# Kernel tuning notes

Hardware: AMD Instinct MI355X
Metric: run time of the kernel (lower is better)

Reference implementation:

```python
import jax, jax.numpy as jnp
import numpy as np

# LIF neuron constants (standard mem_update)
THRESH = 0.5
LENS = 0.5
DECAY = 0.25
EPS = 1e-5
NUM_HEADS = 8

@jax.custom_vjp
def act_fun(mem):
    return (mem > THRESH).astype(mem.dtype)

def _act_fwd(mem):
    return act_fun(mem), mem

def _act_bwd(mem, g):
    surrogate = (jnp.abs(mem - THRESH) < LENS).astype(g.dtype)
    return (g * surrogate,)

act_fun.defvjp(_act_fwd, _act_bwd)

def mem_update(x):
    # x: (T, ...) -> binary spikes (T, ...) via recurrent LIF dynamics
    def step(carry, xt):
        mem_old, spike = carry
        # spike is detached in the reset gate (torch .detach())
        mem = mem_old * DECAY * (1.0 - jax.lax.stop_gradient(spike)) + xt
        s = act_fun(mem)
        return (mem, s), s
    init = (jnp.zeros_like(x[0]), jnp.zeros_like(x[0]))
    _, out = jax.lax.scan(step, init, x)
    return out

def bn(x, gamma, beta, mean, var):
    # inference-mode BatchNorm1d over channel dim of (T,B,C,L)
    inv = gamma / jnp.sqrt(var + EPS)
    return x * inv[None, None, :, None] + (beta - mean * inv)[None, None, :, None]

def setup_inputs() -> dict:
    key = jax.random.key(0)
    ks = jax.random.split(key, 11)
    T, B, C, L = 4, 2, 384, 1024
    s = 1.0 / np.sqrt(C)
    return {
        "x": jax.random.normal(ks[0], (T, B, C, L), jnp.float32),
        "W_w": jax.random.normal(ks[1], (2 * C, C), jnp.float32) * s,
        "bn1_gamma": jax.random.uniform(ks[2], (2 * C,), jnp.float32, 0.5, 1.5),
        "bn1_beta": jax.random.normal(ks[3], (2 * C,), jnp.float32) * 0.1,
        "bn1_mean": jax.random.normal(ks[4], (2 * C,), jnp.float32) * 0.1,
        "bn1_var": jax.random.uniform(ks[5], (2 * C,), jnp.float32, 0.5, 1.5),
        "proj_w": jax.random.normal(ks[6], (C, C), jnp.float32) * s,
        "bn2_gamma": jax.random.uniform(ks[7], (C,), jnp.float32, 0.5, 1.5),
        "bn2_beta": jax.random.normal(ks[8], (C,), jnp.float32) * 0.1,
        "bn2_mean": jax.random.normal(ks[9], (C,), jnp.float32) * 0.1,
        "bn2_var": jax.random.uniform(ks[10], (C,), jnp.float32, 0.5, 1.5),
    }

def reference(x, W_w, bn1_gamma, bn1_beta, bn1_mean, bn1_var, proj_w, bn2_gamma, bn2_beta, bn2_mean, bn2_var):
    T, B, C, L = x.shape
    H = NUM_HEADS
    d = C // H
    x_feat = x
    xs = mem_update(x)                                   # binary spikes (T,B,C,L)
    y = jnp.einsum('oc,tbcl->tbol', W_w, xs)             # 1x1 conv C->2C
    y = bn(y, bn1_gamma, bn1_beta, bn1_mean, bn1_var)
    y = y.reshape(T, B, H, 2 * d, L)
    y1, y2 = y[:, :, :, :d, :], y[:, :, :, d:, :]
    xr = xs.reshape(T, B, H, d, L)
    attn = jnp.einsum('tbhdl,tbhdm->tbhlm', y1, xr)      # (L,L) per head
    attn = mem_update(attn)                              # binary spikes
    out = jnp.einsum('tbhdl,tbhlm->tbhdm', y2, attn)
    out = out.reshape(T, B, C, L)
    out = mem_update(out)
    out = jnp.einsum('oc,tbcl->tbol', proj_w, out)       # Wproj 1x1
    out = bn(out, bn2_gamma, bn2_beta, bn2_mean, bn2_var)
    return out + x_feat
```

## Files before the change

kernel.cpp:

```cpp
#include <hip/hip_runtime.h>

#define T_  4
#define B_  2
#define C_  384
#define L_  1024
#define H_  8
#define C2_ 768
#define S_  (B_*C_*L_)

typedef __attribute__((ext_vector_type(8))) short short8;
typedef __attribute__((ext_vector_type(4))) float floatx4;
typedef __attribute__((ext_vector_type(16))) float floatx16;

__device__ __forceinline__ unsigned bf16_rne(float v) {
    unsigned u = __float_as_uint(v);
    u += 0x7FFFu + ((u >> 16) & 1u);
    return u >> 16;
}
__device__ __forceinline__ float bf16_to_f(unsigned h) { return __uint_as_float(h << 16); }
__device__ __forceinline__ void split3(float v, unsigned& hi, unsigned& mi, unsigned& lo) {
    hi = bf16_rne(v);
    float r1 = v - bf16_to_f(hi);
    mi = bf16_rne(r1);
    float r2 = r1 - bf16_to_f(mi);
    lo = bf16_rne(r2);
}

__global__ __launch_bounds__(256) void split_w(const float* __restrict__ W, int n4,
                                               unsigned short* __restrict__ hi,
                                               unsigned short* __restrict__ mi,
                                               unsigned short* __restrict__ lo) {
    int i = blockIdx.x * 256 + threadIdx.x;
    if (i >= n4) return;
    float4 v = ((const float4*)W)[i];
    float vv[4] = {v.x, v.y, v.z, v.w};
    union { unsigned short us[4]; uint2 u2; } h, m, l;
#pragma unroll
    for (int e = 0; e < 4; e++) {
        unsigned hh, mm, ll; split3(vv[e], hh, mm, ll);
        h.us[e] = (unsigned short)hh; m.us[e] = (unsigned short)mm; l.us[e] = (unsigned short)ll;
    }
    ((uint2*)hi)[i] = h.u2; ((uint2*)mi)[i] = m.u2; ((uint2*)lo)[i] = l.u2;
}

__global__ __launch_bounds__(256) void scan_transpose(const float* __restrict__ src,
                                                      unsigned short* __restrict__ dstT) {
    __shared__ unsigned short tile[64][72];
    const int tid = threadIdx.x;
    const int l0 = blockIdx.x * 64, c0 = blockIdx.y * 64, b = blockIdx.z;
    const int row = tid >> 2, seg = tid & 3;
    float mem[16], sp[16];
#pragma unroll
    for (int e = 0; e < 16; e++) { mem[e] = 0.f; sp[e] = 0.f; }
    for (int t = 0; t < T_; t++) {
        const size_t base = ((size_t)((t*B_ + b)*C_ + c0 + row))*L_ + l0 + seg*16;
#pragma unroll
        for (int qq = 0; qq < 4; qq++) {
            float4 v = *(const float4*)(src + base + qq*4);
            float vv[4] = {v.x, v.y, v.z, v.w};
            unsigned bs[4];
#pragma unroll
            for (int s = 0; s < 4; s++) {
                int e = qq*4 + s;
                mem[e] = mem[e]*0.25f*(1.f - sp[e]) + vv[s];
                bool sb = mem[e] > 0.5f;
                sp[e] = sb ? 1.f : 0.f;
                bs[s] = sb ? 0x3F80u : 0u;
            }
            *(unsigned*)&tile[row][seg*16 + qq*4]     = bs[0] | (bs[1] << 16);
            *(unsigned*)&tile[row][seg*16 + qq*4 + 2] = bs[2] | (bs[3] << 16);
        }
        __syncthreads();
        {
            const int lr = tid >> 2, cs = tid & 3;
#pragma unroll
            for (int sub = 0; sub < 2; sub++) {
                unsigned wv[4];
#pragma unroll
                for (int p = 0; p < 4; p++) {
                    unsigned e0 = tile[cs*16 + sub*8 + p*2][lr];
                    unsigned e1 = tile[cs*16 + sub*8 + p*2 + 1][lr];
                    wv[p] = e0 | (e1 << 16);
                }
                uint4 o; o.x = wv[0]; o.y = wv[1]; o.z = wv[2]; o.w = wv[3];
                *(uint4*)(dstT + ((size_t)(t*B_ + b)*L_ + l0 + lr)*C_ + c0 + cs*16 + sub*8) = o;
            }
        }
        __syncthreads();
    }
}

__global__ __launch_bounds__(256) void gemm1_mfma(
    const unsigned short* __restrict__ whi, const unsigned short* __restrict__ wmi,
    const unsigned short* __restrict__ wlo, const unsigned short* __restrict__ xsT,
    const float* __restrict__ g, const float* __restrict__ be,
    const float* __restrict__ mn, const float* __restrict__ vr,
    unsigned short* __restrict__ y1hi, unsigned short* __restrict__ y1mi,
    unsigned short* __restrict__ y1lo,
    unsigned short* __restrict__ y2hi, unsigned short* __restrict__ y2mi,
    unsigned short* __restrict__ y2lo) {
    __shared__ unsigned short A_hi[96][40], A_mi[96][40], A_lo[96][40];
    __shared__ unsigned short B_s[128][40];
    __shared__ unsigned short epi1[128*56];
    __shared__ unsigned short epi2[48*136];
    const int tid = threadIdx.x;
    const int tb = blockIdx.y;
    const int mt = blockIdx.x >> 3, lt = blockIdx.x & 7;
    const int l0 = lt * 128;
    const int w = tid >> 6, lane = tid & 63;
    const int q = lane >> 4, n15 = lane & 15;
    const int mw = (w & 1) * 48, lw = (w >> 1) * 64;

    floatx4 acc[3][4];
#pragma unroll
    for (int i = 0; i < 3; i++)
#pragma unroll
        for (int j = 0; j < 4; j++) acc[i][j] = (floatx4){0.f,0.f,0.f,0.f};

    for (int ck = 0; ck < C_; ck += 32) {
#pragma unroll
        for (int p = 0; p < 3; p++) {
            const unsigned short* wp = p == 0 ? whi : p == 1 ? wmi : wlo;
            unsigned short (*ap)[40] = p == 0 ? A_hi : p == 1 ? A_mi : A_lo;
            for (int s = tid; s < 384; s += 256) {
                int r = s >> 2, c = s & 3;
                *(uint4*)&ap[r][c*8] = *(const uint4*)(wp + (size_t)(mt*96 + r)*C_ + ck + c*8);
            }
        }
        for (int s = tid; s < 512; s += 256) {
            int r = s >> 2, c4 = s & 3;
            *(uint4*)&B_s[r][c4*8] = *(const uint4*)(xsT + ((size_t)tb*L_ + l0 + r)*C_ + ck + c4*8);
        }
        __syncthreads();
        short8 bb[4];
#pragma unroll
        for (int in = 0; in < 4; in++)
            bb[in] = *(short8*)&B_s[lw + in*16 + n15][q*8];
#pragma unroll
        for (int im = 0; im < 3; im++) {
            short8 ah = *(short8*)&A_hi[mw + im*16 + n15][q*8];
            short8 am = *(short8*)&A_mi[mw + im*16 + n15][q*8];
            short8 al = *(short8*)&A_lo[mw + im*16 + n15][q*8];
#pragma unroll
            for (int in = 0; in < 4; in++) {
                acc[im][in] = __builtin_amdgcn_mfma_f32_16x16x32_bf16(ah, bb[in], acc[im][in], 0,0,0);
                acc[im][in] = __builtin_amdgcn_mfma_f32_16x16x32_bf16(am, bb[in], acc[im][in], 0,0,0);
                acc[im][in] = __builtin_amdgcn_mfma_f32_16x16x32_bf16(al, bb[in], acc[im][in], 0,0,0);
            }
        }
        __syncthreads();
    }

#pragma unroll
    for (int im = 0; im < 3; im++)
#pragma unroll
        for (int r = 0; r < 4; r++) {
            int o = mt*96 + mw + im*16 + q*4 + r;
            float inv = g[o] / sqrtf(vr[o] + 1e-5f);
            float sh = be[o] - mn[o]*inv;
#pragma unroll
            for (int in = 0; in < 4; in++)
                acc[im][in][r] = acc[im][in][r]*inv + sh;
        }
    const bool isY1 = ((w & 1) == 0);
#pragma unroll
    for (int p = 0; p < 3; p++) {
        if (isY1) {
#pragma unroll
            for (int im = 0; im < 3; im++)
#pragma unroll
                for (int in = 0; in < 4; in++) {
                    union { unsigned short us[4]; uint2 u2; } pk;
#pragma unroll
                    for (int r = 0; r < 4; r++) {
                        unsigned hh = bf16_rne(acc[im][in][r]);
                        pk.us[r] = (unsigned short)hh;
                        acc[im][in][r] -= bf16_to_f(hh);
                    }
                    *(uint2*)&epi1[(lw + in*16 + n15)*56 + im*16 + q*4] = pk.u2;
                }
        } else {
#pragma unroll
            for (int im = 0; im < 3; im++)
#pragma unroll
                for (int in = 0; in < 4; in++)
#pragma unroll
                    for (int r = 0; r < 4; r++) {
                        unsigned hh = bf16_rne(acc[im][in][r]);
                        epi2[(im*16 + q*4 + r)*136 + lw + in*16 + n15] = (unsigned short)hh;
                        acc[im][in][r] -= bf16_to_f(hh);
                    }
        }
        __syncthreads();
        unsigned short* y1p = p == 0 ? y1hi : p == 1 ? y1mi : y1lo;
        unsigned short* y2p = p == 0 ? y2hi : p == 1 ? y2mi : y2lo;
#pragma unroll
        for (int k2 = 0; k2 < 3; k2++) {
            int s = tid + k2*256;
            int r1 = s / 6, c8 = s % 6;
            *(uint4*)(y1p + (((size_t)tb*H_ + mt)*L_ + l0 + r1)*48 + c8*8) =
                *(uint4*)&epi1[r1*56 + c8*8];
            int cr = s >> 4, lq = s & 15;
            *(uint4*)(y2p + ((size_t)tb*C_ + mt*48 + cr)*L_ + l0 + lq*8) =
                *(uint4*)&epi2[cr*136 + lq*8];
        }
        __syncthreads();
    }
}

__global__ __launch_bounds__(256) void attn_spike_mfma(
    const unsigned short* __restrict__ y1hi, const unsigned short* __restrict__ y1mi,
    const unsigned short* __restrict__ y1lo, const unsigned short* __restrict__ xsT,
    unsigned* __restrict__ bits) {
    __shared__ unsigned short A_hi[64][56], A_mi[64][56], A_lo[64][56], B_s[64][56];
    __shared__ unsigned bits_s[64][2];
    const int tid = threadIdx.x;
    const int flat = blockIdx.x;
    const int xcd = flat & 7;
    const int ii = flat >> 3;
    const int bh = xcd*2 + (ii >> 8);
    const int rr = ii & 255;
    const int b = bh >> 3, h = bh & 7;
    const int lbase = (rr >> 4)*64, mbase = (rr & 15)*64;
    const int w = tid >> 6, lane = tid & 63;
    const int l31 = lane & 31, half = lane >> 5;
    const int i = w & 1, j = w >> 1;

    float mem[16];
#pragma unroll
    for (int r = 0; r < 16; r++) mem[r] = 0.f;

    for (int t = 0; t < T_; t++) {
        const int tb = t*B_ + b;
        const size_t yb = (((size_t)tb*H_ + h)*L_ + lbase)*48;
        const size_t xb = ((size_t)tb*L_ + mbase)*C_ + h*48;
        for (int s = tid; s < 384; s += 256) {
            int r = s / 6, c = s % 6;
            size_t ro = yb + (size_t)r*48 + c*8;
            *(uint4*)&A_hi[r][c*8] = *(const uint4*)(y1hi + ro);
            *(uint4*)&A_mi[r][c*8] = *(const uint4*)(y1mi + ro);
            *(uint4*)&A_lo[r][c*8] = *(const uint4*)(y1lo + ro);
            *(uint4*)&B_s[r][c*8]  = *(const uint4*)(xsT + xb + (size_t)r*C_ + c*8);
        }
        if (tid < 128) bits_s[tid >> 1][tid & 1] = 0u;
        __syncthreads();

        floatx16 acc = {0.f,0.f,0.f,0.f,0.f,0.f,0.f,0.f,0.f,0.f,0.f,0.f,0.f,0.f,0.f,0.f};
#pragma unroll
        for (int ks = 0; ks < 3; ks++) {
            const int kcol = ks*16 + half*8;
            short8 bb = *(short8*)&B_s[j*32 + l31][kcol];
            short8 ah = *(short8*)&A_hi[i*32 + l31][kcol];
            short8 am = *(short8*)&A_mi[i*32 + l31][kcol];
            short8 al = *(short8*)&A_lo[i*32 + l31][kcol];
            acc = __builtin_amdgcn_mfma_f32_32x32x16_bf16(ah, bb, acc, 0,0,0);
            acc = __builtin_amdgcn_mfma_f32_32x32x16_bf16(am, bb, acc, 0,0,0);
            acc = __builtin_amdgcn_mfma_f32_32x32x16_bf16(al, bb, acc, 0,0,0);
        }

        unsigned word = 0;
#pragma unroll
        for (int r = 0; r < 16; r++) {
            float m = (mem[r] > 0.5f ? 0.f : mem[r]*0.25f) + acc[r];
            mem[r] = m;
            int lloc = (r & 3) + 8*(r >> 2) + 4*half;
            word |= (m > 0.5f) ? (1u << lloc) : 0u;
        }
        atomicOr(&bits_s[j*32 + l31][i], word);
        __syncthreads();
        if (tid < 128) {
            int m = tid >> 1, wd = tid & 1;
            bits[((size_t)(tb*H_ + h)*L_ + mbase + m)*32 + (lbase >> 5) + wd] = bits_s[m][wd];
        }
        __syncthreads();
    }
}

__global__ __launch_bounds__(256) void attn_out_mfma(
    const unsigned short* __restrict__ y2hi, const unsigned short* __restrict__ y2mi,
    const unsigned short* __restrict__ y2lo,
    const unsigned* __restrict__ bits, float* __restrict__ outpre) {
    __shared__ unsigned short A_hi[48][72], A_mi[48][72], A_lo[48][72];
    const int tid = threadIdx.x;
    const int flat = blockIdx.x;
    const int xcd = flat & 7;
    const int ii = flat >> 3;
    const int tbh = xcd*8 + (ii >> 4);
    const int mtile = ii & 15;
    const int t = tbh >> 4, b = (tbh >> 3) & 1, h = tbh & 7;
    const int tb = t*B_ + b;
    const int w = tid >> 6, lane = tid & 63;
    const int q = lane >> 4, n15 = lane & 15;
    const int mb = mtile*64 + w*16;

    floatx4 acc[3];
#pragma unroll
    for (int i = 0; i < 3; i++) acc[i] = (floatx4){0.f,0.f,0.f,0.f};

    const unsigned* brow = bits + ((size_t)(tb*H_ + h)*L_ + mb + n15)*32;
    const size_t y2b = ((size_t)tb*C_ + h*48)*L_;

    for (int lt = 0; lt < L_; lt += 64) {
        for (int s = tid; s < 384; s += 256) {
            int r = s >> 3, c = s & 7;
            size_t ro = y2b + (size_t)r*L_ + lt + c*8;
            *(uint4*)&A_hi[r][c*8] = *(const uint4*)(y2hi + ro);
            *(uint4*)&A_mi[r][c*8] = *(const uint4*)(y2mi + ro);
            *(uint4*)&A_lo[r][c*8] = *(const uint4*)(y2lo + ro);
        }
        uint2 bw = *(const uint2*)(brow + (lt >> 5));
        __syncthreads();
#pragma unroll
        for (int kc = 0; kc < 2; kc++) {
            unsigned word = kc ? bw.y : bw.x;
            unsigned byt = (word >> (q*8)) & 0xFFu;
            union { unsigned u[4]; short8 v; } bu;
#pragma unroll
            for (int p = 0; p < 4; p++)
                bu.u[p] = (((byt >> (2*p)) & 1u) ? 0x3F80u : 0u)
                        | (((byt >> (2*p+1)) & 1u) ? 0x3F800000u : 0u);
            short8 bfrag = bu.v;
#pragma unroll
            for (int i = 0; i < 3; i++) {
                int ra = i*16 + n15;
                short8 ah = *(short8*)&A_hi[ra][kc*32 + q*8];
                short8 am = *(short8*)&A_mi[ra][kc*32 + q*8];
                short8 al = *(short8*)&A_lo[ra][kc*32 + q*8];
                acc[i] = __builtin_amdgcn_mfma_f32_16x16x32_bf16(ah, bfrag, acc[i], 0,0,0);
                acc[i] = __builtin_amdgcn_mfma_f32_16x16x32_bf16(am, bfrag, acc[i], 0,0,0);
                acc[i] = __builtin_amdgcn_mfma_f32_16x16x32_bf16(al, bfrag, acc[i], 0,0,0);
            }
        }
        __syncthreads();
    }
#pragma unroll
    for (int i = 0; i < 3; i++)
#pragma unroll
        for (int r = 0; r < 4; r++) {
            int d = i*16 + q*4 + r;
            outpre[((size_t)tb*C_ + h*48 + d)*L_ + mb + n15] = acc[i][r];
        }
}

__global__ __launch_bounds__(256) void gemm2_mfma(
    const unsigned short* __restrict__ whi, const unsigned short* __restrict__ wmi,
    const unsigned short* __restrict__ wlo, const unsigned short* __restrict__ xT,
    const float* __restrict__ g, const float* __restrict__ be,
    const float* __restrict__ mn, const float* __restrict__ vr,
    const float* __restrict__ res, float* __restrict__ out) {
    __shared__ unsigned short A_hi[96][40], A_mi[96][40], A_lo[96][40];
    __shared__ unsigned short B_s[64][40];
    const int tid = threadIdx.x;
    const int tb = blockIdx.y;
    const int mt = blockIdx.x >> 4, lt = blockIdx.x & 15;
    const int l0 = lt * 64;
    const int w = tid >> 6, lane = tid & 63;
    const int q = lane >> 4, n15 = lane & 15;
    const int mw = (w & 1) * 48, lw = (w >> 1) * 32;

    floatx4 acc[3][2];
#pragma unroll
    for (int i = 0; i < 3; i++)
#pragma unroll
        for (int j = 0; j < 2; j++) acc[i][j] = (floatx4){0.f,0.f,0.f,0.f};

    for (int ck = 0; ck < C_; ck += 32) {
#pragma unroll
        for (int p = 0; p < 3; p++) {
            const unsigned short* wp = p == 0 ? whi : p == 1 ? wmi : wlo;
            unsigned short (*ap)[40] = p == 0 ? A_hi : p == 1 ? A_mi : A_lo;
            for (int s = tid; s < 384; s += 256) {
                int r = s >> 2, c = s & 3;
                *(uint4*)&ap[r][c*8] = *(const uint4*)(wp + (size_t)(mt*96 + r)*C_ + ck + c*8);
            }
        }
        {
            int r = tid >> 2, c4 = tid & 3;
            *(uint4*)&B_s[r][c4*8] = *(const uint4*)(xT + ((size_t)tb*L_ + l0 + r)*C_ + ck + c4*8);
        }
        __syncthreads();
        short8 bb[2];
#pragma unroll
        for (int in = 0; in < 2; in++)
            bb[in] = *(short8*)&B_s[lw + in*16 + n15][q*8];
#pragma unroll
        for (int im = 0; im < 3; im++) {
            short8 ah = *(short8*)&A_hi[mw + im*16 + n15][q*8];
            short8 am = *(short8*)&A_mi[mw + im*16 + n15][q*8];
            short8 al = *(short8*)&A_lo[mw + im*16 + n15][q*8];
#pragma unroll
            for (int in = 0; in < 2; in++) {
                acc[im][in] = __builtin_amdgcn_mfma_f32_16x16x32_bf16(ah, bb[in], acc[im][in], 0,0,0);
                acc[im][in] = __builtin_amdgcn_mfma_f32_16x16x32_bf16(am, bb[in], acc[im][in], 0,0,0);
                acc[im][in] = __builtin_amdgcn_mfma_f32_16x16x32_bf16(al, bb[in], acc[im][in], 0,0,0);
            }
        }
        __syncthreads();
    }
#pragma unroll
    for (int im = 0; im < 3; im++)
#pragma unroll
        for (int r = 0; r < 4; r++) {
            int o = mt*96 + mw + im*16 + q*4 + r;
            float inv = g[o] / sqrtf(vr[o] + 1e-5f);
            float sh = be[o] - mn[o]*inv;
#pragma unroll
            for (int in = 0; in < 2; in++) {
                int l = l0 + lw + in*16 + n15;
                size_t idx = ((size_t)tb*C_ + o)*L_ + l;
                out[idx] = acc[im][in][r]*inv + sh + res[idx];
            }
        }
}

extern "C" void kernel_launch(void* const* d_in, const int* in_sizes, int n_in,
                              void* d_out, int out_size, void* d_ws, size_t ws_size,
                              hipStream_t stream) {
    const float* x   = (const float*)d_in[0];
    const float* W_w = (const float*)d_in[1];
    const float* g1  = (const float*)d_in[2];
    const float* b1  = (const float*)d_in[3];
    const float* m1  = (const float*)d_in[4];
    const float* v1  = (const float*)d_in[5];
    const float* pw  = (const float*)d_in[6];
    const float* g2  = (const float*)d_in[7];
    const float* b2  = (const float*)d_in[8];
    const float* m2  = (const float*)d_in[9];
    const float* v2  = (const float*)d_in[10];

    float* ws = (float*)d_ws;
    unsigned short* xsT  = (unsigned short*)ws;
    unsigned short* y1hi = (unsigned short*)(ws + 1572864);
    unsigned short* y1mi = (unsigned short*)(ws + 3145728);
    unsigned short* y1lo = (unsigned short*)(ws + 4718592);
    unsigned short* y2hi = (unsigned short*)(ws + 6291456);
    unsigned short* y2mi = (unsigned short*)(ws + 7864320);
    unsigned short* y2lo = (unsigned short*)(ws + 9437184);
    unsigned*       bits = (unsigned*)(ws + 11010048);
    unsigned short* wspl[3]  = {(unsigned short*)(ws + 13107200),
                                (unsigned short*)(ws + 13254656),
                                (unsigned short*)(ws + 13402112)};
    unsigned short* pwspl[3] = {(unsigned short*)(ws + 13549568),
                                (unsigned short*)(ws + 13623296),
                                (unsigned short*)(ws + 13697024)};
    float*          outpre = (float*)(ws + 1572864);
    unsigned short* outsT  = (unsigned short*)(ws + 4718592);
    float* out = (float*)d_out;

    split_w<<<dim3(288), 256, 0, stream>>>(W_w, C2_*C_/4, wspl[0], wspl[1], wspl[2]);
    split_w<<<dim3(144), 256, 0, stream>>>(pw,  C_*C_/4, pwspl[0], pwspl[1], pwspl[2]);
    scan_transpose<<<dim3(16, 6, B_), 256, 0, stream>>>(x, xsT);
    gemm1_mfma<<<dim3(64, 8), 256, 0, stream>>>(wspl[0], wspl[1], wspl[2], xsT,
                                                g1, b1, m1, v1,
                                                y1hi, y1mi, y1lo, y2hi, y2mi, y2lo);
    attn_spike_mfma<<<dim3(4096), 256, 0, stream>>>(y1hi, y1mi, y1lo, xsT, bits);
    attn_out_mfma<<<dim3(1024), 256, 0, stream>>>(y2hi, y2mi, y2lo, bits, outpre);
    scan_transpose<<<dim3(16, 6, B_), 256, 0, stream>>>(outpre, outsT);
    gemm2_mfma<<<dim3(64, 8), 256, 0, stream>>>(pwspl[0], pwspl[1], pwspl[2], outsT,
                                                g2, b2, m2, v2, x, out);
}
```

Before: 223.6 us.

## Fuse LIF scan and transpose into attention-output kernel with split-K

The attention-output GEMM now loops over the time dimension inside each block, keeps LIF membrane state in registers, and writes transposed bf16 spikes directly for the projection GEMM. This removes the fp32 outpre round trip through global memory and a separate scan_transpose launch. Blocks grow to 512 threads, with two wave groups splitting K and a shared-memory reduction added. The grid shrinks from 1024 to 256 blocks and each block now runs the four timesteps serially, which may reduce parallelism on a large GPU.

```diff
diff --git a/kernel.cpp b/kernel.cpp
--- a/kernel.cpp
+++ b/kernel.cpp
@@ -276,70 +276,98 @@
     }
 }
 
-__global__ __launch_bounds__(256) void attn_out_mfma(
+__global__ __launch_bounds__(512) void attn_out_scan(
     const unsigned short* __restrict__ y2hi, const unsigned short* __restrict__ y2mi,
     const unsigned short* __restrict__ y2lo,
-    const unsigned* __restrict__ bits, float* __restrict__ outpre) {
-    __shared__ unsigned short A_hi[48][72], A_mi[48][72], A_lo[48][72];
+    const unsigned* __restrict__ bits, unsigned short* __restrict__ outsT) {
+    __shared__ unsigned short A_hi[48][136], A_mi[48][136], A_lo[48][136];
+    __shared__ float red[4][48][17];
+    __shared__ unsigned short epi[64][48];
     const int tid = threadIdx.x;
     const int flat = blockIdx.x;
-    const int xcd = flat & 7;
-    const int ii = flat >> 3;
-    const int tbh = xcd*8 + (ii >> 4);
-    const int mtile = ii & 15;
-    const int t = tbh >> 4, b = (tbh >> 3) & 1, h = tbh & 7;
-    const int tb = t*B_ + b;
+    const int xcd = flat & 7, ii = flat >> 3;
+    const int bh = xcd*2 + (ii >> 4), mtile = ii & 15;
+    const int b = bh >> 3, h = bh & 7;
     const int w = tid >> 6, lane = tid & 63;
     const int q = lane >> 4, n15 = lane & 15;
-    const int mb = mtile*64 + w*16;
-
-    floatx4 acc[3];
-#pragma unroll
-    for (int i = 0; i < 3; i++) acc[i] = (floatx4){0.f,0.f,0.f,0.f};
-
-    const unsigned* brow = bits + ((size_t)(tb*H_ + h)*L_ + mb + n15)*32;
-    const size_t y2b = ((size_t)tb*C_ + h*48)*L_;
-
-    for (int lt = 0; lt < L_; lt += 64) {
-        for (int s = tid; s < 384; s += 256) {
-            int r = s >> 3, c = s & 7;
-            size_t ro = y2b + (size_t)r*L_ + lt + c*8;
-            *(uint4*)&A_hi[r][c*8] = *(const uint4*)(y2hi + ro);
-            *(uint4*)&A_mi[r][c*8] = *(const uint4*)(y2mi + ro);
-            *(uint4*)&A_lo[r][c*8] = *(const uint4*)(y2lo + ro);
-        }
-        uint2 bw = *(const uint2*)(brow + (lt >> 5));
-        __syncthreads();
-#pragma unroll
-        for (int kc = 0; kc < 2; kc++) {
-            unsigned word = kc ? bw.y : bw.x;
-            unsigned byt = (word >> (q*8)) & 0xFFu;
-            union { unsigned u[4]; short8 v; } bu;
-#pragma unroll
-            for (int p = 0; p < 4; p++)
-                bu.u[p] = (((byt >> (2*p)) & 1u) ? 0x3F80u : 0u)
-                        | (((byt >> (2*p+1)) & 1u) ? 0x3F800000u : 0u);
-            short8 bfrag = bu.v;
-#pragma unroll
-            for (int i = 0; i < 3; i++) {
-                int ra = i*16 + n15;
-                short8 ah = *(short8*)&A_hi[ra][kc*32 + q*8];
-                short8 am = *(short8*)&A_mi[ra][kc*32 + q*8];
-                short8 al = *(short8*)&A_lo[ra][kc*32 + q*8];
-                acc[i] = __builtin_amdgcn_mfma_f32_16x16x32_bf16(ah, bfrag, acc[i], 0,0,0);
-                acc[i] = __builtin_amdgcn_mfma_f32_16x16x32_bf16(am, bfrag, acc[i], 0,0,0);
-                acc[i] = __builtin_amdgcn_mfma_f32_16x16x32_bf16(al, bfrag, acc[i], 0,0,0);
-            }
-        }
-        __syncthreads();
-    }
+    const int mq = w & 3, lh = w >> 2;
+    const int mb = mtile*64 + mq*16;
+
+    float mem[3][4];
 #pragma unroll
     for (int i = 0; i < 3; i++)
 #pragma unroll
-        for (int r = 0; r < 4; r++) {
-            int d = i*16 + q*4 + r;
-            outpre[((size_t)tb*C_ + h*48 + d)*L_ + mb + n15] = acc[i][r];
-        }
+        for (int r = 0; r < 4; r++) mem[i][r] = 0.f;
+
+    for (int t = 0; t < T_; t++) {
+        const int tb = t*B_ + b;
+        const size_t y2b = ((size_t)tb*C_ + h*48)*L_;
+        const unsigned* brow = bits + ((size_t)(tb*H_ + h)*L_ + mb + n15)*32;
+        floatx4 acc[3];
+#pragma unroll
+        for (int i = 0; i < 3; i++) acc[i] = (floatx4){0.f,0.f,0.f,0.f};
+
+        for (int kb = 0; kb < 8; kb++) {
+            for (int s = tid; s < 768; s += 512) {
+                int r = s >> 4, c = s & 15;
+                size_t ro = y2b + (size_t)r*L_ + kb*128 + c*8;
+                *(uint4*)&A_hi[r][c*8] = *(const uint4*)(y2hi + ro);
+                *(uint4*)&A_mi[r][c*8] = *(const uint4*)(y2mi + ro);
+                *(uint4*)&A_lo[r][c*8] = *(const uint4*)(y2lo + ro);
+            }
+            uint2 bw = *(const uint2*)(brow + kb*4 + lh*2);
+            __syncthreads();
+#pragma unroll
+            for (int kc = 0; kc < 2; kc++) {
+                unsigned word = kc ? bw.y : bw.x;
+                unsigned byt = (word >> (q*8)) & 0xFFu;
+                union { unsigned u[4]; short8 v; } bu;
+#pragma unroll
+                for (int p = 0; p < 4; p++)
+                    bu.u[p] = (((byt >> (2*p)) & 1u) ? 0x3F80u : 0u)
+                            | (((byt >> (2*p+1)) & 1u) ? 0x3F800000u : 0u);
+                short8 bfrag = bu.v;
+                const int col = lh*64 + kc*32 + q*8;
+#pragma unroll
+                for (int i = 0; i < 3; i++) {
+                    int ra = i*16 + n15;
+                    short8 ah = *(short8*)&A_hi[ra][col];
+                    short8 am = *(short8*)&A_mi[ra][col];
+                    short8 al = *(short8*)&A_lo[ra][col];
+                    acc[i] = __builtin_amdgcn_mfma_f32_16x16x32_bf16(ah, bfrag, acc[i], 0,0,0);
+                    acc[i] = __builtin_amdgcn_mfma_f32_16x16x32_bf16(am, bfrag, acc[i], 0,0,0);
+                    acc[i] = __builtin_amdgcn_mfma_f32_16x16x32_bf16(al, bfrag, acc[i], 0,0,0);
+                }
+            }
+            __syncthreads();
+        }
+        if (lh == 1) {
+#pragma unroll
+            for (int i = 0; i < 3; i++)
+#pragma unroll
+                for (int r = 0; r < 4; r++)
+                    red[mq][i*16 + q*4 + r][n15] = acc[i][r];
+        }
+        __syncthreads();
+        if (lh == 0) {
+#pragma unroll
+            for (int i = 0; i < 3; i++)
+#pragma unroll
+                for (int r = 0; r < 4; r++) {
+                    float v = acc[i][r] + red[mq][i*16 + q*4 + r][n15];
+                    float m = (mem[i][r] > 0.5f ? 0.f : mem[i][r]*0.25f) + v;
+                    mem[i][r] = m;
+                    epi[mq*16 + n15][i*16 + q*4 + r] = (m > 0.5f) ? 0x3F80u : 0u;
+                }
+        }
+        __syncthreads();
+        for (int s = tid; s < 384; s += 512) {
+            int r = s / 6, c = s % 6;
+            *(uint4*)(outsT + ((size_t)tb*L_ + mtile*64 + r)*C_ + h*48 + c*8) =
+                *(uint4*)&epi[r][c*8];
+        }
+        __syncthreads();
+    }
 }
 
 __global__ __launch_bounds__(256) void gemm2_mfma(
@@ -443,7 +471,6 @@
     unsigned short* pwspl[3] = {(unsigned short*)(ws + 13549568),
                                 (unsigned short*)(ws + 13623296),
                                 (unsigned short*)(ws + 13697024)};
-    float*          outpre = (float*)(ws + 1572864);
     unsigned short* outsT  = (unsigned short*)(ws + 4718592);
     float* out = (float*)d_out;
 
@@ -454,8 +481,7 @@
                                                 g1, b1, m1, v1,
                                                 y1hi, y1mi, y1lo, y2hi, y2mi, y2lo);
     attn_spike_mfma<<<dim3(4096), 256, 0, stream>>>(y1hi, y1mi, y1lo, xsT, bits);
-    attn_out_mfma<<<dim3(1024), 256, 0, stream>>>(y2hi, y2mi, y2lo, bits, outpre);
-    scan_transpose<<<dim3(16, 6, B_), 256, 0, stream>>>(outpre, outsT);
+    attn_out_scan<<<dim3(256), 512, 0, stream>>>(y2hi, y2mi, y2lo, bits, outsT);
     gemm2_mfma<<<dim3(64, 8), 256, 0, stream>>>(pwspl[0], pwspl[1], pwspl[2], outsT,
                                                 g2, b2, m2, v2, x, out);
 }
```

Result: slower. 239.0 us (+6.8%).
